# Performance work log

Measured on AMD Instinct MI355X. Metric: run time of the kernel, lower is better.

## Reference

```python
import jax, jax.numpy as jnp
import numpy as np

B, S, D, H = 4, 2048, 1024, 16
HD = D // H


def setup_inputs() -> dict:
    key = jax.random.key(0)
    k1, k2, k3 = jax.random.split(key, 3)
    x = jax.random.normal(k1, (B, S, D), dtype=jnp.float32)
    W_qkv = jax.random.normal(k2, (D, 3 * D), dtype=jnp.float32) * (1.0 / np.sqrt(D))
    b_qkv = jnp.zeros((3 * D,), dtype=jnp.float32)
    W_out = jax.random.normal(k3, (D, D), dtype=jnp.float32) * (1.0 / np.sqrt(D))
    b_out = jnp.zeros((D,), dtype=jnp.float32)
    return {"x": x, "W_qkv": W_qkv, "b_qkv": b_qkv, "W_out": W_out, "b_out": b_out}


def reference(x, W_qkv, b_qkv, W_out, b_out):
    b, s, d = x.shape
    qkv = x @ W_qkv + b_qkv                      # [B,S,3D]
    q, k, v = jnp.split(qkv, 3, axis=-1)
    # split heads: [B,S,D] -> [B,H,S,HD]
    def split_heads(t):
        return t.reshape(b, s, H, HD).transpose(0, 2, 1, 3)
    q, k, v = split_heads(q), split_heads(k), split_heads(v)
    scale = jnp.sqrt(jnp.asarray(HD, jnp.float32))
    scores = jnp.einsum('bhqd,bhkd->bhqk', q, k) / scale  # [B,H,S,S]
    # causal mask exactly as in the original: scores*mask + (1-mask)*(-1e9)
    mask = jnp.tril(jnp.ones((s, s), dtype=scores.dtype))[None, None]
    scores = scores * mask + (1.0 - mask) * (-1e9)
    weights = jax.nn.softmax(scores, axis=-1)
    # dropout is identity at inference (training=False)
    attn = jnp.einsum('bhqk,bhkd->bhqd', weights, v)      # [B,H,S,HD]
    attn = attn.transpose(0, 2, 1, 3).reshape(b, s, d)    # merge heads
    return attn @ W_out + b_out
```

## Files before the change

### kernel.cpp

```cpp
#include <hip/hip_runtime.h>
#include <hip/hip_bf16.h>


typedef float f32x4 __attribute__((ext_vector_type(4)));
typedef short bf16x8 __attribute__((ext_vector_type(8)));

__device__ __forceinline__ ushort f2b(float f) {
  unsigned int x = __float_as_uint(f);
  unsigned int r = (x + 0x7fffu + ((x >> 16) & 1u)) >> 16;
  return (ushort)r;
}
__device__ __forceinline__ float b2f(ushort u) {
  return __uint_as_float(((unsigned int)u) << 16);
}
__device__ __forceinline__ float exp2fast(float x) {
#if __has_builtin(__builtin_amdgcn_exp2f)
  return __builtin_amdgcn_exp2f(x);
#else
  return __expf(x * 0.69314718055994531f);
#endif
}

__global__ void detect_dtype(const unsigned int* __restrict__ x, int* __restrict__ flag) {
  __shared__ int cnt;
  if (threadIdx.x == 0) cnt = 0;
  __syncthreads();
  unsigned int w = x[threadIdx.x];
  int e = (w >> 7) & 0xff;
  atomicAdd(&cnt, (e >= 96 && e <= 160) ? 1 : 0);
  __syncthreads();
  if (threadIdx.x == 0) flag[0] = (cnt >= 614) ? 1 : 0;
}

__global__ void transpose_two(const void* __restrict__ in1, ushort* __restrict__ out1,
                              int N1, const void* __restrict__ in2,
                              ushort* __restrict__ out2, int N2, int xsplit,
                              const int* __restrict__ flag) {
  __shared__ ushort tile[64][65];
  int bf = flag[0];
  const void* in;
  ushort* out;
  int N, bx;
  if ((int)blockIdx.x < xsplit) {
    in = in1; out = out1; N = N1; bx = blockIdx.x;
  } else {
    in = in2; out = out2; N = N2; bx = blockIdx.x - xsplit;
  }
  const int K = 1024;
  int k0 = blockIdx.y * 64, n0 = bx * 64;
  int t = threadIdx.x;
#pragma unroll
  for (int i = 0; i < 16; ++i) {
    int idx = i * 256 + t;
    int r = idx >> 6, c = idx & 63;
    size_t g = (size_t)(k0 + r) * N + (n0 + c);
    tile[r][c] = bf ? ((const ushort*)in)[g] : f2b(((const float*)in)[g]);
  }
  __syncthreads();
#pragma unroll
  for (int i = 0; i < 16; ++i) {
    int idx = i * 256 + t;
    int r = idx >> 6, c = idx & 63;
    out[(size_t)(n0 + r) * K + (k0 + c)] = tile[c][r];
  }
}

#define BM 128
#define BN 128
#define BKK 32
#define LDB 32

__global__ void gemm_bt(const void* __restrict__ A, const ushort* __restrict__ BT,
                        const void* __restrict__ bias, void* __restrict__ C,
                        int M, int N, int K, int lda, size_t a_off, size_t c_off,
                        const int* __restrict__ flag, int a_is_input, int c_is_output) {
  __shared__ __align__(16) ushort As[BM * LDB];
  __shared__ __align__(16) ushort Bs[BN * LDB];
  int bf = flag[0];
  int a_bf = a_is_input ? bf : 1;
  int tid = threadIdx.x;
  int wave = tid >> 6, lane = tid & 63;
  int lrow = lane & 15, quad = lane >> 4;
  int m0 = blockIdx.y * BM, n0 = blockIdx.x * BN;
  int wm = (wave >> 1) * 64, wn = (wave & 1) * 64;

  f32x4 acc[4][4] = {};

  const ushort* Bp = BT + (size_t)n0 * K;
  int srow = lane >> 2;
  int scol = (lane & 3) << 3;

  for (int kt = 0; kt < K; kt += BKK) {
    __syncthreads();
    if (a_bf) {
#pragma unroll
      for (int j = 0; j < 2; ++j) {
        int seg = j * 4 + wave;
        const ushort* gp = (const ushort*)A + a_off +
                           (size_t)(m0 + seg * 16 + srow) * lda + kt + scol;
        __builtin_amdgcn_global_load_lds(
            (const __attribute__((address_space(1))) void*)gp,
            (__attribute__((address_space(3))) void*)&As[seg * 16 * LDB], 16, 0, 0);
      }
    } else {
#pragma unroll
      for (int j = 0; j < 2; ++j) {
        int seg = j * 4 + wave;
        int r = seg * 16 + srow;
        const float* Af = (const float*)A + a_off + (size_t)(m0 + r) * lda + kt + scol;
        float4 f0 = *(const float4*)Af;
        float4 f1 = *(const float4*)(Af + 4);
        ushort tmp[8] = {f2b(f0.x), f2b(f0.y), f2b(f0.z), f2b(f0.w),
                         f2b(f1.x), f2b(f1.y), f2b(f1.z), f2b(f1.w)};
        *(uint4*)&As[r * LDB + scol] = *(const uint4*)tmp;
      }
    }
#pragma unroll
    for (int j = 0; j < 2; ++j) {
      int seg = j * 4 + wave;
      const ushort* gp = Bp + (size_t)(seg * 16 + srow) * K + kt + scol;
      __builtin_amdgcn_global_load_lds(
          (const __attribute__((address_space(1))) void*)gp,
          (__attribute__((address_space(3))) void*)&Bs[seg * 16 * LDB], 16, 0, 0);
    }
    __syncthreads();

    bf16x8 af[4], bfr[4];
#pragma unroll
    for (int i = 0; i < 4; ++i) {
      af[i] = *(const bf16x8*)&As[(wm + i * 16 + lrow) * LDB + quad * 8];
      bfr[i] = *(const bf16x8*)&Bs[(wn + i * 16 + lrow) * LDB + quad * 8];
    }
#pragma unroll
    for (int i = 0; i < 4; ++i)
#pragma unroll
      for (int j = 0; j < 4; ++j)
        acc[i][j] = __builtin_amdgcn_mfma_f32_16x16x32_bf16(af[i], bfr[j], acc[i][j], 0, 0, 0);
  }

#pragma unroll
  for (int i = 0; i < 4; ++i) {
#pragma unroll
    for (int j = 0; j < 4; ++j) {
      int colg = n0 + wn + j * 16 + lrow;
      float bvs = bf ? b2f(((const ushort*)bias)[colg]) : ((const float*)bias)[colg];
#pragma unroll
      for (int r = 0; r < 4; ++r) {
        int rowg = m0 + wm + i * 16 + quad * 4 + r;
        float val = acc[i][j][r] + bvs;
        size_t ci = c_off + (size_t)rowg * N + colg;
        if (c_is_output && !bf)
          ((float*)C)[ci] = val;
        else
          ((ushort*)C)[ci] = f2b(val);
      }
    }
  }
}

__global__ void gemm_bt64(const ushort* __restrict__ A, const ushort* __restrict__ BT,
                          const void* __restrict__ bias, void* __restrict__ C,
                          int N, int K, int lda, size_t c_off,
                          const int* __restrict__ flag) {
  __shared__ __align__(16) ushort As[BM * LDB];
  __shared__ __align__(16) ushort Bs[64 * LDB];
  int bf = flag[0];
  int tid = threadIdx.x;
  int wave = tid >> 6, lane = tid & 63;
  int lrow = lane & 15, quad = lane >> 4;
  int m0 = blockIdx.y * BM, n0 = blockIdx.x * 64;
  int wm = (wave >> 1) * 64, wn = (wave & 1) * 32;

  f32x4 acc[4][2] = {};

  const ushort* Bp = BT + (size_t)n0 * K;
  int srow = lane >> 2;
  int scol = (lane & 3) << 3;

  for (int kt = 0; kt < K; kt += BKK) {
    __syncthreads();
#pragma unroll
    for (int j = 0; j < 2; ++j) {
      int seg = j * 4 + wave;
      const ushort* gp = A + (size_t)(m0 + seg * 16 + srow) * lda + kt + scol;
      __builtin_amdgcn_global_load_lds(
          (const __attribute__((address_space(1))) void*)gp,
          (__attribute__((address_space(3))) void*)&As[seg * 16 * LDB], 16, 0, 0);
    }
    {
      int seg = wave;
      const ushort* gp = Bp + (size_t)(seg * 16 + srow) * K + kt + scol;
      __builtin_amdgcn_global_load_lds(
          (const __attribute__((address_space(1))) void*)gp,
          (__attribute__((address_space(3))) void*)&Bs[seg * 16 * LDB], 16, 0, 0);
    }
    __syncthreads();

    bf16x8 af[4], bfr[2];
#pragma unroll
    for (int i = 0; i < 4; ++i)
      af[i] = *(const bf16x8*)&As[(wm + i * 16 + lrow) * LDB + quad * 8];
#pragma unroll
    for (int j = 0; j < 2; ++j)
      bfr[j] = *(const bf16x8*)&Bs[(wn + j * 16 + lrow) * LDB + quad * 8];
#pragma unroll
    for (int i = 0; i < 4; ++i)
#pragma unroll
      for (int j = 0; j < 2; ++j)
        acc[i][j] = __builtin_amdgcn_mfma_f32_16x16x32_bf16(af[i], bfr[j], acc[i][j], 0, 0, 0);
  }

#pragma unroll
  for (int i = 0; i < 4; ++i) {
#pragma unroll
    for (int j = 0; j < 2; ++j) {
      int colg = n0 + wn + j * 16 + lrow;
      float bvs = bf ? b2f(((const ushort*)bias)[colg]) : ((const float*)bias)[colg];
#pragma unroll
      for (int r = 0; r < 4; ++r) {
        int rowg = m0 + wm + i * 16 + quad * 4 + r;
        float val = acc[i][j][r] + bvs;
        size_t ci = c_off + (size_t)rowg * N + colg;
        if (!bf)
          ((float*)C)[ci] = val;
        else
          ((ushort*)C)[ci] = f2b(val);
      }
    }
  }
}

#define LDK 72

__global__ void attn_mfma(ushort* __restrict__ qkv_all) {
  __shared__ __align__(16) ushort Ks[64 * LDK];
  __shared__ __align__(16) ushort Vs[64 * LDK];

  int flat = blockIdx.x + 32 * blockIdx.y + 512 * blockIdx.z;
  int qt = 31 - (flat >> 5);
  int h = flat & 15;
  int z = (flat >> 4) & 1;

  ushort* qkv = qkv_all + (size_t)z * 2048 * 3072;
  int q0 = qt * 64;
  int tid = threadIdx.x, wave = tid >> 6, lane = tid & 63;
  int lrow = lane & 15, quad = lane >> 4;

  bf16x8 qa[2];
#pragma unroll
  for (int kk = 0; kk < 2; ++kk)
    qa[kk] = *(const bf16x8*)(qkv + (size_t)(q0 + wave * 16 + lrow) * 3072 +
                              h * 64 + kk * 32 + quad * 8);

  f32x4 o[4] = {};
  float li = 0.f;
  const float SCALE2 = 0.125f * 1.44269504089f;
  int qg = q0 + wave * 16 + lrow;

  int ntiles = qt + 1;

  uint4 kv[2], vv[2];
#pragma unroll
  for (int j = 0; j < 2; ++j) {
    int idx = j * 256 + tid;
    {
      int r = idx >> 3;
      int c = (idx & 7) << 3;
      kv[j] = *(const uint4*)(qkv + (size_t)r * 3072 + 1024 + h * 64 + c);
    }
    {
      int hd = idx & 63;
      int kb = idx >> 6;
      const ushort* vg = qkv + (size_t)(kb * 8) * 3072 + 2048 + h * 64 + hd;
      __align__(16) ushort col[8];
#pragma unroll
      for (int e = 0; e < 8; ++e) col[e] = vg[(size_t)e * 3072];
      vv[j] = *(const uint4*)col;
    }
  }

  for (int kt = 0; kt < ntiles; ++kt) {
    __syncthreads();
#pragma unroll
    for (int j = 0; j < 2; ++j) {
      int idx = j * 256 + tid;
      int r = idx >> 3;
      int c = (idx & 7) << 3;
      *(uint4*)&Ks[r * LDK + c] = kv[j];
      int hd = idx & 63;
      int kb = idx >> 6;
      *(uint4*)&Vs[hd * LDK + kb * 8] = vv[j];
    }
    __syncthreads();

    if (kt + 1 < ntiles) {
#pragma unroll
      for (int j = 0; j < 2; ++j) {
        int idx = j * 256 + tid;
        {
          int r = idx >> 3;
          int c = (idx & 7) << 3;
          kv[j] = *(const uint4*)(qkv + (size_t)((kt + 1) * 64 + r) * 3072 + 1024 + h * 64 + c);
        }
        {
          int hd = idx & 63;
          int kb = idx >> 6;
          const ushort* vg = qkv + (size_t)((kt + 1) * 64 + kb * 8) * 3072 + 2048 + h * 64 + hd;
          __align__(16) ushort col[8];
#pragma unroll
          for (int e = 0; e < 8; ++e) col[e] = vg[(size_t)e * 3072];
          vv[j] = *(const uint4*)col;
        }
      }
    }

    f32x4 s4[4];
    __builtin_amdgcn_s_setprio(1);
#pragma unroll
    for (int t = 0; t < 4; ++t) {
      f32x4 a = {};
#pragma unroll
      for (int kk = 0; kk < 2; ++kk) {
        bf16x8 kb = *(const bf16x8*)&Ks[(t * 16 + lrow) * LDK + kk * 32 + quad * 8];
        a = __builtin_amdgcn_mfma_f32_16x16x32_bf16(kb, qa[kk], a, 0, 0, 0);
      }
      s4[t] = a;
    }
    __builtin_amdgcn_s_setprio(0);

#pragma unroll
    for (int t = 0; t < 4; ++t) {
      int keyb = kt * 64 + t * 16 + quad * 4;
#pragma unroll
      for (int r = 0; r < 4; ++r) {
        float v = s4[t][r] * SCALE2;
        if (keyb + r > qg) v = -1e30f;
        float p = exp2fast(v);
        s4[t][r] = p;
        li += p;
      }
    }

    unsigned d[4][2];
#pragma unroll
    for (int t = 0; t < 4; ++t) {
      asm("v_cvt_pk_bf16_f32 %0, %1, %2" : "=v"(d[t][0]) : "v"(s4[t][0]), "v"(s4[t][1]));
      asm("v_cvt_pk_bf16_f32 %0, %1, %2" : "=v"(d[t][1]) : "v"(s4[t][2]), "v"(s4[t][3]));
    }

    int srcA = ((quad & 1) << 5) | lrow;
    int srcB = srcA + 16;
    bool thi = (quad & 2) != 0;
    bf16x8 pa[2];
#pragma unroll
    for (int kk = 0; kk < 2; ++kk) {
      unsigned a0 = d[2 * kk][0], a1 = d[2 * kk][1];
      unsigned b0 = d[2 * kk + 1][0], b1 = d[2 * kk + 1][1];
      unsigned xa0 = __shfl(a0, srcA, 64), xa1 = __shfl(a1, srcA, 64);
      unsigned xb0 = __shfl(b0, srcA, 64), xb1 = __shfl(b1, srcA, 64);
      unsigned ya0 = __shfl(a0, srcB, 64), ya1 = __shfl(a1, srcB, 64);
      unsigned yb0 = __shfl(b0, srcB, 64), yb1 = __shfl(b1, srcB, 64);
      __align__(16) unsigned w[4];
      w[0] = thi ? xb0 : xa0;
      w[1] = thi ? xb1 : xa1;
      w[2] = thi ? yb0 : ya0;
      w[3] = thi ? yb1 : ya1;
      pa[kk] = *(const bf16x8*)w;
    }

    __builtin_amdgcn_s_setprio(1);
#pragma unroll
    for (int t = 0; t < 4; ++t)
#pragma unroll
      for (int kk = 0; kk < 2; ++kk) {
        bf16x8 vb = *(const bf16x8*)&Vs[(t * 16 + lrow) * LDK + kk * 32 + quad * 8];
        o[t] = __builtin_amdgcn_mfma_f32_16x16x32_bf16(pa[kk], vb, o[t], 0, 0, 0);
      }
    __builtin_amdgcn_s_setprio(0);
  }

  li += __shfl_xor(li, 16, 64);
  li += __shfl_xor(li, 32, 64);

  int sbase = quad * 20;
  float lir[4];
#pragma unroll
  for (int r = 0; r < 4; ++r) lir[r] = __shfl(li, sbase + r, 64);
#pragma unroll
  for (int r = 0; r < 4; ++r) {
    float inv = 1.f / lir[r];
    int q = q0 + wave * 16 + quad * 4 + r;
    size_t base = (size_t)q * 3072 + h * 64;
#pragma unroll
    for (int t = 0; t < 4; ++t) qkv[base + t * 16 + lrow] = f2b(o[t][r] * inv);
  }
}

static const void* ptr_by_size(void* const* d_in, const int* in_sizes, int n_in,
                               int want, int fallback_idx) {
  for (int i = 0; i < n_in; ++i)
    if (in_sizes[i] == want) return d_in[i];
  return d_in[fallback_idx];
}

extern "C" void kernel_launch(void* const* d_in, const int* in_sizes, int n_in,
                              void* d_out, int out_size, void* d_ws, size_t ws_size,
                              hipStream_t stream) {
  const void* x    = ptr_by_size(d_in, in_sizes, n_in, 8388608, 0);
  const void* Wqkv = ptr_by_size(d_in, in_sizes, n_in, 3145728, 1);
  const void* bqkv = ptr_by_size(d_in, in_sizes, n_in, 3072,    2);
  const void* Wout = ptr_by_size(d_in, in_sizes, n_in, 1048576, 3);
  const void* bout = ptr_by_size(d_in, in_sizes, n_in, 1024,    4);

  char* ws = (char*)d_ws;
  int*    flag  = (int*)ws;
  ushort* WT1   = (ushort*)(ws + 256);
  ushort* WT2   = (ushort*)(ws + 256 + 6291456);
  ushort* qkvb  = (ushort*)(ws + 256 + 8388608);

  detect_dtype<<<1, 1024, 0, stream>>>((const unsigned int*)x, flag);
  transpose_two<<<dim3(64, 16), 256, 0, stream>>>(Wqkv, WT1, 3072, Wout, WT2, 1024,
                                                  48, flag);

  for (int p = 0; p < 2; ++p) {
    gemm_bt<<<dim3(24, 32), 256, 0, stream>>>(
        x, WT1, bqkv, qkvb, 4096, 3072, 1024, 1024,
        (size_t)p * 4096 * 1024, 0, flag, 1, 0);
    attn_mfma<<<dim3(32, 16, 2), 256, 0, stream>>>(qkvb);
    gemm_bt64<<<dim3(16, 32), 256, 0, stream>>>(
        qkvb, WT2, bout, d_out, 1024, 1024, 3072,
        (size_t)p * 4096 * 1024, flag);
  }
}
```

Baseline: 404.4 us.

## Use 128-query attention blocks with 8 waves sharing each K/V tile

Each attention workgroup now has 512 threads (8 waves) covering 128 query rows instead of 64. Every 64-key K/V tile staged in LDS is shared by twice as many waves, and each thread loads one K and one V chunk per tile instead of two. This roughly halves the global and LDS staging traffic per query. In exchange, the lower half of each block walks one extra mostly-masked key tile, and the grid has half as many larger blocks, which can worsen causal load balance.

```diff
diff --git a/kernel.cpp b/kernel.cpp
--- a/kernel.cpp
+++ b/kernel.cpp
@@ -236,82 +236,67 @@
   __shared__ __align__(16) ushort Ks[64 * LDK];
   __shared__ __align__(16) ushort Vs[64 * LDK];
 
-  int flat = blockIdx.x + 32 * blockIdx.y + 512 * blockIdx.z;
-  int qt = 31 - (flat >> 5);
+  int flat = blockIdx.x + 16 * blockIdx.y + 256 * blockIdx.z;
+  int qt = 15 - (flat >> 5);
   int h = flat & 15;
   int z = (flat >> 4) & 1;
 
   ushort* qkv = qkv_all + (size_t)z * 2048 * 3072;
-  int q0 = qt * 64;
+  int q0 = qt * 128;
   int tid = threadIdx.x, wave = tid >> 6, lane = tid & 63;
   int lrow = lane & 15, quad = lane >> 4;
+  int wrow0 = q0 + wave * 16;
 
   bf16x8 qa[2];
 #pragma unroll
   for (int kk = 0; kk < 2; ++kk)
-    qa[kk] = *(const bf16x8*)(qkv + (size_t)(q0 + wave * 16 + lrow) * 3072 +
+    qa[kk] = *(const bf16x8*)(qkv + (size_t)(wrow0 + lrow) * 3072 +
                               h * 64 + kk * 32 + quad * 8);
 
   f32x4 o[4] = {};
   float li = 0.f;
   const float SCALE2 = 0.125f * 1.44269504089f;
-  int qg = q0 + wave * 16 + lrow;
-
-  int ntiles = qt + 1;
-
-  uint4 kv[2], vv[2];
-#pragma unroll
-  for (int j = 0; j < 2; ++j) {
-    int idx = j * 256 + tid;
+  int qg = wrow0 + lrow;
+
+  int ntiles = 2 * qt + 2;
+
+  uint4 kv, vv;
+  {
+    int r = tid >> 3;
+    int c = (tid & 7) << 3;
+    kv = *(const uint4*)(qkv + (size_t)r * 3072 + 1024 + h * 64 + c);
+    int hd = tid & 63;
+    int kb = tid >> 6;
+    const ushort* vg = qkv + (size_t)(kb * 8) * 3072 + 2048 + h * 64 + hd;
+    __align__(16) ushort col[8];
+#pragma unroll
+    for (int e = 0; e < 8; ++e) col[e] = vg[(size_t)e * 3072];
+    vv = *(const uint4*)col;
+  }
+
+  for (int kt = 0; kt < ntiles; ++kt) {
+    __syncthreads();
     {
-      int r = idx >> 3;
-      int c = (idx & 7) << 3;
-      kv[j] = *(const uint4*)(qkv + (size_t)r * 3072 + 1024 + h * 64 + c);
-    }
-    {
-      int hd = idx & 63;
-      int kb = idx >> 6;
-      const ushort* vg = qkv + (size_t)(kb * 8) * 3072 + 2048 + h * 64 + hd;
+      int r = tid >> 3;
+      int c = (tid & 7) << 3;
+      *(uint4*)&Ks[r * LDK + c] = kv;
+      int hd = tid & 63;
+      int kb = tid >> 6;
+      *(uint4*)&Vs[hd * LDK + kb * 8] = vv;
+    }
+    __syncthreads();
+
+    if (kt + 1 < ntiles) {
+      int r = tid >> 3;
+      int c = (tid & 7) << 3;
+      kv = *(const uint4*)(qkv + (size_t)((kt + 1) * 64 + r) * 3072 + 1024 + h * 64 + c);
+      int hd = tid & 63;
+      int kb = tid >> 6;
+      const ushort* vg = qkv + (size_t)((kt + 1) * 64 + kb * 8) * 3072 + 2048 + h * 64 + hd;
       __align__(16) ushort col[8];
 #pragma unroll
       for (int e = 0; e < 8; ++e) col[e] = vg[(size_t)e * 3072];
-      vv[j] = *(const uint4*)col;
-    }
-  }
-
-  for (int kt = 0; kt < ntiles; ++kt) {
-    __syncthreads();
-#pragma unroll
-    for (int j = 0; j < 2; ++j) {
-      int idx = j * 256 + tid;
-      int r = idx >> 3;
-      int c = (idx & 7) << 3;
-      *(uint4*)&Ks[r * LDK + c] = kv[j];
-      int hd = idx & 63;
-      int kb = idx >> 6;
-      *(uint4*)&Vs[hd * LDK + kb * 8] = vv[j];
-    }
-    __syncthreads();
-
-    if (kt + 1 < ntiles) {
-#pragma unroll
-      for (int j = 0; j < 2; ++j) {
-        int idx = j * 256 + tid;
-        {
-          int r = idx >> 3;
-          int c = (idx & 7) << 3;
-          kv[j] = *(const uint4*)(qkv + (size_t)((kt + 1) * 64 + r) * 3072 + 1024 + h * 64 + c);
-        }
-        {
-          int hd = idx & 63;
-          int kb = idx >> 6;
-          const ushort* vg = qkv + (size_t)((kt + 1) * 64 + kb * 8) * 3072 + 2048 + h * 64 + hd;
-          __align__(16) ushort col[8];
-#pragma unroll
-          for (int e = 0; e < 8; ++e) col[e] = vg[(size_t)e * 3072];
-          vv[j] = *(const uint4*)col;
-        }
-      }
+      vv = *(const uint4*)col;
     }
 
     f32x4 s4[4];
@@ -389,7 +374,7 @@
 #pragma unroll
   for (int r = 0; r < 4; ++r) {
     float inv = 1.f / lir[r];
-    int q = q0 + wave * 16 + quad * 4 + r;
+    int q = wrow0 + quad * 4 + r;
     size_t base = (size_t)q * 3072 + h * 64;
 #pragma unroll
     for (int t = 0; t < 4; ++t) qkv[base + t * 16 + lrow] = f2b(o[t][r] * inv);
@@ -426,7 +411,7 @@
     gemm_bt<<<dim3(24, 32), 256, 0, stream>>>(
         x, WT1, bqkv, qkvb, 4096, 3072, 1024, 1024,
         (size_t)p * 4096 * 1024, 0, flag, 1, 0);
-    attn_mfma<<<dim3(32, 16, 2), 256, 0, stream>>>(qkvb);
+    attn_mfma<<<dim3(16, 16, 2), 512, 0, stream>>>(qkvb);
     gemm_bt64<<<dim3(16, 32), 256, 0, stream>>>(
         qkvb, WT2, bout, d_out, 1024, 1024, 3072,
         (size_t)p * 4096 * 1024, flag);
```

Result: faster. 363.3 us (-10.2%).
